# Kernel optimization log

Measured on AMD Instinct MI355X. Metric: run time of the kernel, lower is better.

The kernel has to match this reference:

```python
import jax, jax.numpy as jnp
import numpy as np

N_NODES = 100000
N_EDGES = 1600000
F_IN, F_HID, F_OUT = 512, 128, 64


def add_self_loops(edge_index, num_nodes):
    loop = jnp.arange(num_nodes, dtype=edge_index.dtype)
    loops = jnp.stack([loop, loop])  # [2, N]
    return jnp.concatenate([edge_index, loops], axis=1)


def gcn_conv(x, edge_index_sl, W, b, num_nodes):
    # x: [N, F_in], edge_index_sl: [2, E+N] (self-loops included)
    h = x @ W  # [N, F_out] transform before propagation (PyG GCNConv order)
    src, dst = edge_index_sl[0], edge_index_sl[1]
    ones = jnp.ones(src.shape[0], dtype=h.dtype)
    deg = jax.ops.segment_sum(ones, dst, num_segments=num_nodes)  # in-degree w/ self-loops
    dinv = jnp.where(deg > 0, jax.lax.rsqrt(deg), 0.0)
    norm = dinv[src] * dinv[dst]  # [E+N] symmetric normalization
    msg = h[src] * norm[:, None]  # gather + scale
    out = jax.ops.segment_sum(msg, dst, num_segments=num_nodes)  # scatter-add
    return out + b


def setup_inputs() -> dict:
    key = jax.random.key(0)
    k = jax.random.split(key, 6)
    x = jax.random.normal(k[0], (N_NODES, F_IN), dtype=jnp.float32)
    edge_index = jax.random.randint(k[1], (2, N_EDGES), 0, N_NODES, dtype=jnp.int64)
    W1 = jax.random.normal(k[2], (F_IN, F_HID), dtype=jnp.float32) * (1.0 / np.sqrt(F_IN))
    b1 = jnp.zeros((F_HID,), dtype=jnp.float32)
    W2 = jax.random.normal(k[3], (F_HID, F_OUT), dtype=jnp.float32) * (1.0 / np.sqrt(F_HID))
    b2 = jnp.zeros((F_OUT,), dtype=jnp.float32)
    return {"x": x, "edge_index": edge_index, "W1": W1, "b1": b1, "W2": W2, "b2": b2}


def reference(x, edge_index, W1, b1, W2, b2):
    ei = add_self_loops(edge_index, N_NODES)
    h = jax.nn.relu(gcn_conv(x, ei, W1, b1, N_NODES))
    out = gcn_conv(h, ei, W2, b2, N_NODES)
    return out
```

## Files before the change

### kernel.cpp

```cpp
#include <hip/hip_runtime.h>

#define N_NODES 100000
#define N_EDGES 1600000
#define F_IN 512
#define F_HID 128
#define F_OUT 64

#define BSH 8
#define NBUK 391

typedef unsigned int u32;
typedef __attribute__((ext_vector_type(8))) short bf16x8;
typedef __attribute__((ext_vector_type(4))) float f32x4;

__device__ float g7_bf2f(unsigned short u) {
    return __uint_as_float(((unsigned int)u) << 16);
}

__device__ unsigned short g7_f2bf(float f) {
    unsigned int u = __float_as_uint(f);
    u = u + 0x7fffu + ((u >> 16) & 1u);
    return (unsigned short)(u >> 16);
}

__device__ float2 g7_up(unsigned int u) {
    float2 r;
    r.x = __uint_as_float(u << 16);
    r.y = __uint_as_float(u & 0xffff0000u);
    return r;
}

__device__ static inline void g7_gl2lds16(const void* g, void* l) {
    __builtin_amdgcn_global_load_lds(
        (const __attribute__((address_space(1))) u32*)g,
        (__attribute__((address_space(3))) u32*)l, 16, 0, 0);
}

__global__ void GCN_16716012716713_kernel() {}

__global__ void g7_zero(int* p, int n) {
    int i = blockIdx.x * blockDim.x + threadIdx.x;
    if (i < n) p[i] = 0;
}

__global__ void g7_iprobe(const int* raw, int* iflag) {
    __shared__ int s[256];
    int tid = threadIdx.x;
    int f = 0;
    for (int i = tid; i < 1024; i += 256) {
        if (raw[2 * i + 1] != 0) f = 1;
    }
    s[tid] = f;
    __syncthreads();
    for (int off = 128; off > 0; off >>= 1) {
        if (tid < off) s[tid] |= s[tid + off];
        __syncthreads();
    }
    if (tid == 0) iflag[0] = s[0];
}

__global__ void g7_fprobe(const unsigned int* xw, int* fflag) {
    __shared__ int s[256];
    int tid = threadIdx.x;
    int cnt = 0;
    for (int i = tid; i < 4096; i += 256) {
        unsigned int lo = xw[i] & 0xffffu;
        unsigned int e = (lo >> 7) & 0xffu;
        if (e >= 110u && e <= 140u) cnt = cnt + 1;
    }
    s[tid] = cnt;
    __syncthreads();
    for (int off = 128; off > 0; off >>= 1) {
        if (tid < off) s[tid] += s[tid + off];
        __syncthreads();
    }
    if (tid == 0) fflag[0] = (s[0] > 2048) ? 1 : 0;
}

__global__ void g7_pack(const int* raw, const int* iflag, int* ei, int* deg) {
    int i = blockIdx.x * blockDim.x + threadIdx.x;
    if (i < 2 * N_EDGES) {
        int v;
        if (iflag[0] == 0) {
            v = raw[2 * i];
        } else {
            v = raw[i];
        }
        ei[i] = v;
        if (i >= N_EDGES) atomicAdd(&deg[v], 1);
    }
}

__global__ void g7_prep(const void* W1, const void* W2, const void* b1, const void* b2,
                        const int* fflag, unsigned short* W1Th, unsigned short* W1Tl,
                        float* W2f, float* b1f, float* b2f) {
    int i = blockIdx.x * blockDim.x + threadIdx.x;
    int isbf = fflag[0];
    if (i < F_IN * F_HID) {
        int k = i >> 7;
        int n = i & 127;
        float w;
        if (isbf == 1) {
            w = g7_bf2f(((const unsigned short*)W1)[i]);
        } else {
            w = ((const float*)W1)[i];
        }
        unsigned short hi = g7_f2bf(w);
        unsigned short lo = g7_f2bf(w - g7_bf2f(hi));
        W1Th[n * F_IN + k] = hi;
        W1Tl[n * F_IN + k] = lo;
    } else if (i < F_IN * F_HID + F_HID * F_OUT) {
        int j = i - F_IN * F_HID;
        W2f[j] = (isbf == 1) ? g7_bf2f(((const unsigned short*)W2)[j])
                             : ((const float*)W2)[j];
    } else if (i < F_IN * F_HID + F_HID * F_OUT + F_HID) {
        int j = i - F_IN * F_HID - F_HID * F_OUT;
        b1f[j] = (isbf == 1) ? g7_bf2f(((const unsigned short*)b1)[j])
                             : ((const float*)b1)[j];
    } else if (i < F_IN * F_HID + F_HID * F_OUT + F_HID + F_OUT) {
        int j = i - F_IN * F_HID - F_HID * F_OUT - F_HID;
        b2f[j] = (isbf == 1) ? g7_bf2f(((const unsigned short*)b2)[j])
                             : ((const float*)b2)[j];
    }
}

__global__ void g7_dinv(const int* deg, float* dinv) {
    int i = blockIdx.x * blockDim.x + threadIdx.x;
    if (i < N_NODES) {
        dinv[i] = rsqrtf((float)deg[i] + 1.0f);
    }
}

__global__ void g7_bsum(const int* deg, int* bsum) {
    __shared__ int s[256];
    int i = blockIdx.x * 256 + threadIdx.x;
    s[threadIdx.x] = (i < N_NODES) ? deg[i] : 0;
    __syncthreads();
    for (int off = 128; off > 0; off >>= 1) {
        if (threadIdx.x < off) s[threadIdx.x] += s[threadIdx.x + off];
        __syncthreads();
    }
    if (threadIdx.x == 0) bsum[blockIdx.x] = s[0];
}

__global__ void g7_bscan(const int* bsum, int* boff, int nblk, int* rowptr) {
    __shared__ int s[512];
    int tid = threadIdx.x;
    int v = (tid < nblk) ? bsum[tid] : 0;
    s[tid] = v;
    __syncthreads();
    for (int off = 1; off < 512; off <<= 1) {
        int t = (tid >= off) ? s[tid - off] : 0;
        __syncthreads();
        s[tid] += t;
        __syncthreads();
    }
    if (tid < nblk) boff[tid] = s[tid] - v;
    if (tid == nblk - 1) rowptr[N_NODES] = s[tid];
}

__global__ void g7_scan(const int* deg, const int* boff, int* rowptr) {
    __shared__ int s[256];
    int i = blockIdx.x * 256 + threadIdx.x;
    int v = (i < N_NODES) ? deg[i] : 0;
    s[threadIdx.x] = v;
    __syncthreads();
    for (int off = 1; off < 256; off <<= 1) {
        int t = (threadIdx.x >= off) ? s[threadIdx.x - off] : 0;
        __syncthreads();
        s[threadIdx.x] += t;
        __syncthreads();
    }
    if (i < N_NODES) {
        rowptr[i] = s[threadIdx.x] - v + boff[blockIdx.x];
    }
}

__global__ void g7_binit(const int* rowptr, int* bcur) {
    int b = blockIdx.x * blockDim.x + threadIdx.x;
    if (b < NBUK) bcur[b] = rowptr[b << BSH];
}

#define P1_EPT 32
#define P1_TILE (256 * P1_EPT)
__global__ void g7_part1(const int* ei, int* bcur, uint2* part) {
    __shared__ int cnt[NBUK + 1];
    __shared__ int base[NBUK + 1];
    int tid = threadIdx.x;
    long long t0 = (long long)blockIdx.x * P1_TILE;
    for (int i = tid; i < NBUK; i += 256) cnt[i] = 0;
    __syncthreads();
#pragma unroll 4
    for (int r = 0; r < P1_EPT; ++r) {
        long long e = t0 + r * 256 + tid;
        if (e < N_EDGES) {
            int d = ei[N_EDGES + e];
            atomicAdd(&cnt[d >> BSH], 1);
        }
    }
    __syncthreads();
    for (int i = tid; i < NBUK; i += 256) {
        int c = cnt[i];
        base[i] = (c > 0) ? atomicAdd(&bcur[i], c) : 0;
        cnt[i] = 0;
    }
    __syncthreads();
#pragma unroll 4
    for (int r = 0; r < P1_EPT; ++r) {
        long long e = t0 + r * 256 + tid;
        if (e < N_EDGES) {
            int s = ei[e];
            int d = ei[N_EDGES + e];
            int bk = d >> BSH;
            int off = atomicAdd(&cnt[bk], 1);
            uint2 p; p.x = (u32)s; p.y = (u32)d;
            part[(long long)base[bk] + off] = p;
        }
    }
}

__global__ void g7_part2(const int* rowptr, const uint2* part, int* csr) {
    __shared__ int lcur[256];
    int b = blockIdx.x;
    int tid = threadIdx.x;
    int n0 = b << BSH;
    int n1 = n0 + 256; if (n1 > N_NODES) n1 = N_NODES;
    if (tid < 256) {
        int node = n0 + tid;
        lcur[tid] = (node < N_NODES) ? rowptr[node] : 0;
    }
    __syncthreads();
    int beg = rowptr[n0];
    int end = rowptr[n1];
    for (int j = beg + tid; j < end; j += 512) {
        uint2 p = part[j];
        int pos = atomicAdd(&lcur[p.y - n0], 1);
        csr[pos] = (int)p.x;
    }
}

__global__ __launch_bounds__(512, 4) void g7_gemm1s(const void* x, const int* fflag,
        const unsigned short* W1Th, const unsigned short* W1Tl, unsigned short* h1b) {
    __shared__ uint4 smv[4096];
    char* smc = (char*)smv;
    int tid = threadIdx.x;
    int m0 = blockIdx.x * 128;
    int w = tid >> 6;
    int lane = tid & 63;
    int wr = w >> 2, wc = w & 3;
    int la = lane & 15;
    int lk = lane >> 4;
    int isbf = fflag[0];
    int ar = tid >> 2;
    int ah = tid & 3;

    f32x4 acc[4][2];
#pragma unroll
    for (int i = 0; i < 4; ++i)
#pragma unroll
        for (int j = 0; j < 2; ++j) acc[i][j] = (f32x4){0.f, 0.f, 0.f, 0.f};

    uint4 rA[2];

    auto loadA = [&](int k0) {
        int m = m0 + ar;
        if (m >= N_NODES) m = N_NODES - 1;
        if (isbf) {
            const char* s = (const char*)x + ((long long)m * F_IN + k0 + ah * 8) * 2;
            rA[0] = *(const uint4*)s;
        } else {
            const char* s = (const char*)x + ((long long)m * F_IN + k0 + ah * 8) * 4;
            rA[0] = *(const uint4*)s;
            rA[1] = *(const uint4*)(s + 16);
        }
    };

    auto writeA = [&](char* As) {
        float f[8];
        if (isbf) {
            const unsigned short* p = (const unsigned short*)&rA[0];
#pragma unroll
            for (int j = 0; j < 8; ++j) f[j] = g7_bf2f(p[j]);
        } else {
            const float* p = (const float*)rA;
#pragma unroll
            for (int j = 0; j < 8; ++j) f[j] = p[j];
        }
        unsigned int hw[4], lw[4];
#pragma unroll
        for (int j = 0; j < 4; ++j) {
            unsigned short h0 = g7_f2bf(f[2 * j]);
            unsigned short h1v = g7_f2bf(f[2 * j + 1]);
            unsigned short l0 = g7_f2bf(f[2 * j] - g7_bf2f(h0));
            unsigned short l1 = g7_f2bf(f[2 * j + 1] - g7_bf2f(h1v));
            hw[j] = (unsigned int)h0 | ((unsigned int)h1v << 16);
            lw[j] = (unsigned int)l0 | ((unsigned int)l1 << 16);
        }
        int swz = (ar & 7) << 4;
        char* dst = As + ar * 128;
        *(uint4*)(dst + ((ah * 16) ^ swz))      = make_uint4(hw[0], hw[1], hw[2], hw[3]);
        *(uint4*)(dst + ((64 + ah * 16) ^ swz)) = make_uint4(lw[0], lw[1], lw[2], lw[3]);
    };

    auto stageB = [&](char* Bs, int k0) {
#pragma unroll
        for (int p = 0; p < 2; ++p) {
            int nr = w * 16 + p * 8 + (lane >> 3);
            int cp = ((lane & 7) * 16) ^ (((lane >> 3) & 7) << 4);
            const char* src = (cp < 64)
                ? (const char*)W1Th + (long long)nr * 1024 + k0 * 2 + cp
                : (const char*)W1Tl + (long long)nr * 1024 + k0 * 2 + (cp - 64);
            g7_gl2lds16(src, Bs + (w * 16 + p * 8) * 128);
        }
    };

    auto compute = [&](const char* As, const char* Bs) {
        bf16x8 bh[2], bl[2];
#pragma unroll
        for (int j = 0; j < 2; ++j) {
            int n = wc * 32 + j * 16 + la;
            int swzb = (n & 7) << 4;
            const char* bb = Bs + n * 128;
            bh[j] = *(const bf16x8*)(bb + ((lk * 16) ^ swzb));
            bl[j] = *(const bf16x8*)(bb + ((64 + lk * 16) ^ swzb));
        }
#pragma unroll
        for (int i = 0; i < 4; ++i) {
            int r = wr * 64 + i * 16 + la;
            int swz = (r & 7) << 4;
            const char* ab = As + r * 128;
            bf16x8 ah_ = *(const bf16x8*)(ab + ((lk * 16) ^ swz));
            bf16x8 al_ = *(const bf16x8*)(ab + ((64 + lk * 16) ^ swz));
#pragma unroll
            for (int j = 0; j < 2; ++j) {
                acc[i][j] = __builtin_amdgcn_mfma_f32_16x16x32_bf16(
                    ah_, bh[j], acc[i][j], 0, 0, 0);
                acc[i][j] = __builtin_amdgcn_mfma_f32_16x16x32_bf16(
                    al_, bh[j], acc[i][j], 0, 0, 0);
                acc[i][j] = __builtin_amdgcn_mfma_f32_16x16x32_bf16(
                    ah_, bl[j], acc[i][j], 0, 0, 0);
            }
        }
    };

    loadA(0);
    stageB(smc + 16384, 0);
    writeA(smc);
    __syncthreads();

    for (int kt = 0; kt < 16; ++kt) {
        char* bc = smc + (kt & 1) * 32768;
        char* bn = smc + ((kt & 1) ^ 1) * 32768;
        if (kt < 15) {
            loadA((kt + 1) * 32);
            stageB(bn + 16384, (kt + 1) * 32);
        }
        compute(bc, bc + 16384);
        if (kt < 15) writeA(bn);
        __syncthreads();
    }

#pragma unroll
    for (int i = 0; i < 4; ++i) {
#pragma unroll
        for (int j = 0; j < 2; ++j) {
            int n = wc * 32 + j * 16 + la;
#pragma unroll
            for (int q = 0; q < 4; ++q) {
                int m = m0 + wr * 64 + i * 16 + lk * 4 + q;
                if (m < N_NODES) {
                    h1b[(long long)m * F_HID + n] = g7_f2bf(acc[i][j][q]);
                }
            }
        }
    }
}

__global__ void g7_agg1(const int* rowptr, const int* csr, const float* dinv,
                        const unsigned short* h1b, const float* b1, float* r1) {
    int node = blockIdx.x * 4 + (threadIdx.x >> 6);
    int lane = threadIdx.x & 63;
    int g = lane >> 4;
    int fl = lane & 15;
    if (node >= N_NODES) return;
    int beg = rowptr[node];
    int end = rowptr[node + 1];
    const uint4* hv = (const uint4*)h1b;
    float a[8];
#pragma unroll
    for (int t = 0; t < 8; ++t) a[t] = 0.f;
    int j = beg + g;
    for (; j + 4 < end; j += 8) {
        int s0 = csr[j];
        int s1 = csr[j + 4];
        float w0 = dinv[s0];
        float w1 = dinv[s1];
        uint4 v0 = hv[(long long)s0 * 16 + fl];
        uint4 v1 = hv[(long long)s1 * 16 + fl];
        float2 p;
        p = g7_up(v0.x); a[0] += p.x * w0; a[1] += p.y * w0;
        p = g7_up(v0.y); a[2] += p.x * w0; a[3] += p.y * w0;
        p = g7_up(v0.z); a[4] += p.x * w0; a[5] += p.y * w0;
        p = g7_up(v0.w); a[6] += p.x * w0; a[7] += p.y * w0;
        p = g7_up(v1.x); a[0] += p.x * w1; a[1] += p.y * w1;
        p = g7_up(v1.y); a[2] += p.x * w1; a[3] += p.y * w1;
        p = g7_up(v1.z); a[4] += p.x * w1; a[5] += p.y * w1;
        p = g7_up(v1.w); a[6] += p.x * w1; a[7] += p.y * w1;
    }
    if (j < end) {
        int s0 = csr[j];
        float w0 = dinv[s0];
        uint4 v0 = hv[(long long)s0 * 16 + fl];
        float2 p;
        p = g7_up(v0.x); a[0] += p.x * w0; a[1] += p.y * w0;
        p = g7_up(v0.y); a[2] += p.x * w0; a[3] += p.y * w0;
        p = g7_up(v0.z); a[4] += p.x * w0; a[5] += p.y * w0;
        p = g7_up(v0.w); a[6] += p.x * w0; a[7] += p.y * w0;
    }
    float di = dinv[node];
    if (g == 0) {
        uint4 vd = hv[(long long)node * 16 + fl];
        float2 p;
        p = g7_up(vd.x); a[0] += p.x * di; a[1] += p.y * di;
        p = g7_up(vd.y); a[2] += p.x * di; a[3] += p.y * di;
        p = g7_up(vd.z); a[4] += p.x * di; a[5] += p.y * di;
        p = g7_up(vd.w); a[6] += p.x * di; a[7] += p.y * di;
    }
#pragma unroll
    for (int t = 0; t < 8; ++t) {
        a[t] += __shfl_xor(a[t], 16);
        a[t] += __shfl_xor(a[t], 32);
    }
    if (g == 0) {
        float4 b0 = *(const float4*)(b1 + 8 * fl);
        float4 b1v = *(const float4*)(b1 + 8 * fl + 4);
        float o[8];
        o[0] = a[0] * di + b0.x; o[1] = a[1] * di + b0.y;
        o[2] = a[2] * di + b0.z; o[3] = a[3] * di + b0.w;
        o[4] = a[4] * di + b1v.x; o[5] = a[5] * di + b1v.y;
        o[6] = a[6] * di + b1v.z; o[7] = a[7] * di + b1v.w;
#pragma unroll
        for (int t = 0; t < 8; ++t) if (o[t] < 0.f) o[t] = 0.f;
        float* dst = r1 + (long long)node * F_HID + 8 * fl;
        float4 s0; s0.x = o[0]; s0.y = o[1]; s0.z = o[2]; s0.w = o[3];
        float4 s1; s1.x = o[4]; s1.y = o[5]; s1.z = o[6]; s1.w = o[7];
        *(float4*)dst = s0;
        *(float4*)(dst + 4) = s1;
    }
}

__global__ void g7_gemm2(const float* r1, const float* W2, unsigned short* h2b) {
    __shared__ float Rs[32][68];
    __shared__ float Ws[32][64];
    int tid = threadIdx.x;
    int m0 = blockIdx.x * 64;
    int tx = tid & 15;
    int ty = tid >> 4;
    float acc[4][4];
#pragma unroll
    for (int i = 0; i < 4; ++i) {
#pragma unroll
        for (int j = 0; j < 4; ++j) acc[i][j] = 0.0f;
    }

    for (int k0 = 0; k0 < F_HID; k0 += 32) {
#pragma unroll
        for (int r = 0; r < 8; ++r) {
            int i = r * 256 + tid;
            int kk = i & 31;
            int mm = i >> 5;
            int m = m0 + mm;
            float v = 0.0f;
            if (m < N_NODES) {
                v = r1[(long long)m * F_HID + k0 + kk];
            }
            Rs[kk][mm] = v;
        }
#pragma unroll
        for (int r = 0; r < 8; ++r) {
            int i = r * 256 + tid;
            int wk = i >> 6;
            int wn = i & 63;
            Ws[wk][wn] = W2[(k0 + wk) * F_OUT + wn];
        }
        __syncthreads();
#pragma unroll
        for (int k = 0; k < 32; ++k) {
            float a[4];
            float b[4];
#pragma unroll
            for (int i = 0; i < 4; ++i) a[i] = Rs[k][ty * 4 + i];
#pragma unroll
            for (int j = 0; j < 4; ++j) b[j] = Ws[k][tx * 4 + j];
#pragma unroll
            for (int i = 0; i < 4; ++i) {
#pragma unroll
                for (int j = 0; j < 4; ++j) acc[i][j] += a[i] * b[j];
            }
        }
        __syncthreads();
    }
#pragma unroll
    for (int i = 0; i < 4; ++i) {
        int m = m0 + ty * 4 + i;
        if (m < N_NODES) {
            unsigned int w0 = (unsigned int)g7_f2bf(acc[i][0])
                            | ((unsigned int)g7_f2bf(acc[i][1]) << 16);
            unsigned int w1 = (unsigned int)g7_f2bf(acc[i][2])
                            | ((unsigned int)g7_f2bf(acc[i][3]) << 16);
            uint2 o; o.x = w0; o.y = w1;
            *(uint2*)(h2b + (long long)m * F_OUT + tx * 4) = o;
        }
    }
}

__global__ void g7_agg2(const int* rowptr, const int* csr, const float* dinv,
                        const unsigned short* h2b, const float* b2, const int* fflag,
                        void* out) {
    int node = blockIdx.x * 4 + (threadIdx.x >> 6);
    int lane = threadIdx.x & 63;
    int g = lane >> 3;
    int fl = lane & 7;
    if (node >= N_NODES) return;
    int beg = rowptr[node];
    int end = rowptr[node + 1];
    const uint4* hv = (const uint4*)h2b;
    float a[8];
#pragma unroll
    for (int t = 0; t < 8; ++t) a[t] = 0.f;
    int j = beg + g;
    for (; j + 8 < end; j += 16) {
        int s0 = csr[j];
        int s1 = csr[j + 8];
        float w0 = dinv[s0];
        float w1 = dinv[s1];
        uint4 v0 = hv[(long long)s0 * 8 + fl];
        uint4 v1 = hv[(long long)s1 * 8 + fl];
        float2 p;
        p = g7_up(v0.x); a[0] += p.x * w0; a[1] += p.y * w0;
        p = g7_up(v0.y); a[2] += p.x * w0; a[3] += p.y * w0;
        p = g7_up(v0.z); a[4] += p.x * w0; a[5] += p.y * w0;
        p = g7_up(v0.w); a[6] += p.x * w0; a[7] += p.y * w0;
        p = g7_up(v1.x); a[0] += p.x * w1; a[1] += p.y * w1;
        p = g7_up(v1.y); a[2] += p.x * w1; a[3] += p.y * w1;
        p = g7_up(v1.z); a[4] += p.x * w1; a[5] += p.y * w1;
        p = g7_up(v1.w); a[6] += p.x * w1; a[7] += p.y * w1;
    }
    if (j < end) {
        int s0 = csr[j];
        float w0 = dinv[s0];
        uint4 v0 = hv[(long long)s0 * 8 + fl];
        float2 p;
        p = g7_up(v0.x); a[0] += p.x * w0; a[1] += p.y * w0;
        p = g7_up(v0.y); a[2] += p.x * w0; a[3] += p.y * w0;
        p = g7_up(v0.z); a[4] += p.x * w0; a[5] += p.y * w0;
        p = g7_up(v0.w); a[6] += p.x * w0; a[7] += p.y * w0;
    }
    float di = dinv[node];
    if (g == 0) {
        uint4 vd = hv[(long long)node * 8 + fl];
        float2 p;
        p = g7_up(vd.x); a[0] += p.x * di; a[1] += p.y * di;
        p = g7_up(vd.y); a[2] += p.x * di; a[3] += p.y * di;
        p = g7_up(vd.z); a[4] += p.x * di; a[5] += p.y * di;
        p = g7_up(vd.w); a[6] += p.x * di; a[7] += p.y * di;
    }
#pragma unroll
    for (int t = 0; t < 8; ++t) {
        a[t] += __shfl_xor(a[t], 8);
        a[t] += __shfl_xor(a[t], 16);
        a[t] += __shfl_xor(a[t], 32);
    }
    if (g == 0) {
        float o[8];
#pragma unroll
        for (int t = 0; t < 8; ++t) o[t] = a[t] * di + b2[8 * fl + t];
        long long oi = (long long)node * F_OUT + 8 * fl;
        if (fflag[0] == 1) {
            unsigned int w0 = (u32)g7_f2bf(o[0]) | ((u32)g7_f2bf(o[1]) << 16);
            unsigned int w1 = (u32)g7_f2bf(o[2]) | ((u32)g7_f2bf(o[3]) << 16);
            unsigned int w2 = (u32)g7_f2bf(o[4]) | ((u32)g7_f2bf(o[5]) << 16);
            unsigned int w3 = (u32)g7_f2bf(o[6]) | ((u32)g7_f2bf(o[7]) << 16);
            *(uint4*)((unsigned short*)out + oi) = make_uint4(w0, w1, w2, w3);
        } else {
            float* dst = (float*)out + oi;
            float4 s0; s0.x = o[0]; s0.y = o[1]; s0.z = o[2]; s0.w = o[3];
            float4 s1; s1.x = o[4]; s1.y = o[5]; s1.z = o[6]; s1.w = o[7];
            *(float4*)dst = s0;
            *(float4*)(dst + 4) = s1;
        }
    }
}

extern "C" void kernel_launch(void* const* d_in, const int* in_sizes, int n_in,
                              void* d_out, int out_size, void* d_ws, size_t ws_size,
                              hipStream_t stream) {
    const void* x     = d_in[0];
    const int* ei_raw = (const int*)d_in[1];
    const void* W1    = d_in[2];
    const void* b1    = d_in[3];
    const void* W2    = d_in[4];
    const void* b2    = d_in[5];

    const int NBLK = (N_NODES + 255) / 256;

    char* ws = (char*)d_ws;
    int*   deg    = (int*)(ws + 0);
    int*   iflag  = (int*)(ws + 409600);
    int*   fflag  = (int*)(ws + 409616);
    int*   bsum   = (int*)(ws + 409632);
    int*   boff   = (int*)(ws + 412800);
    int*   bcur   = (int*)(ws + 450560);
    float* dinv   = (float*)(ws + 524288);
    unsigned short* W1Th = (unsigned short*)(ws + 1048576);
    unsigned short* W1Tl = (unsigned short*)(ws + 1179648);
    float* b1f    = (float*)(ws + 1310720);
    float* W2f    = (float*)(ws + 1311232);
    float* b2f    = (float*)(ws + 1344000);
    int*   ei     = (int*)(ws + 2097152);
    int*   rowptr = (int*)(ws + 14897152);
    int*   csr    = (int*)(ws + 16777216);
    unsigned short* h1b = (unsigned short*)(ws + 23177216);
    uint2* part   = (uint2*)(ws + 50331648);
    float* r1     = (float*)(ws + 74377216);
    unsigned short* h2b = (unsigned short*)(ws + 125577216);

    g7_zero<<<(N_NODES + 255) / 256, 256, 0, stream>>>(deg, N_NODES);

    g7_iprobe<<<1, 256, 0, stream>>>(ei_raw, iflag);
    g7_fprobe<<<1, 256, 0, stream>>>((const unsigned int*)x, fflag);

    g7_pack<<<(2 * N_EDGES + 255) / 256, 256, 0, stream>>>(ei_raw, iflag, ei, deg);

    const int PREP_N = F_IN * F_HID + F_HID * F_OUT + F_HID + F_OUT;
    g7_prep<<<(PREP_N + 255) / 256, 256, 0, stream>>>(W1, W2, b1, b2, fflag,
                                                      W1Th, W1Tl, W2f, b1f, b2f);

    g7_dinv<<<(N_NODES + 255) / 256, 256, 0, stream>>>(deg, dinv);

    g7_bsum<<<NBLK, 256, 0, stream>>>(deg, bsum);
    g7_bscan<<<1, 512, 0, stream>>>(bsum, boff, NBLK, rowptr);
    g7_scan<<<NBLK, 256, 0, stream>>>(deg, boff, rowptr);

    g7_binit<<<(NBUK + 255) / 256, 256, 0, stream>>>(rowptr, bcur);
    g7_part1<<<(N_EDGES + P1_TILE - 1) / P1_TILE, 256, 0, stream>>>(ei, bcur, part);
    g7_part2<<<NBUK, 512, 0, stream>>>(rowptr, part, csr);

    g7_gemm1s<<<(N_NODES + 127) / 128, 512, 0, stream>>>(x, fflag, W1Th, W1Tl, h1b);

    g7_agg1<<<N_NODES / 4, 256, 0, stream>>>(rowptr, csr, dinv, h1b, b1f, r1);

    g7_gemm2<<<(N_NODES + 63) / 64, 256, 0, stream>>>(r1, W2f, h2b);

    g7_agg2<<<N_NODES / 4, 256, 0, stream>>>(rowptr, csr, dinv, h2b, b2f, fflag, d_out);
}
```

Before: 609.3 us.

## Move second GEMM onto MFMA with split-bf16 operands and double-buffered LDS

Replaces the scalar FP32 shared-memory tiled GEMM for layer 2 with an MFMA 16x16x32 bf16 kernel. It splits both operands into hi/lo bf16 parts and uses three MFMAs to keep close to fp32 accuracy. W2 is now pre-transposed and split in the prep kernel, A tiles are converted in registers and written to swizzled LDS, and the K loop is double-buffered with async global-to-LDS loads for B. The output store becomes scalar 16-bit writes, which may be less coalesced than the old vector stores.

```diff
diff --git a/kernel.cpp b/kernel.cpp
--- a/kernel.cpp
+++ b/kernel.cpp
@@ -93,7 +93,8 @@
 
 __global__ void g7_prep(const void* W1, const void* W2, const void* b1, const void* b2,
                         const int* fflag, unsigned short* W1Th, unsigned short* W1Tl,
-                        float* W2f, float* b1f, float* b2f) {
+                        unsigned short* W2Th, unsigned short* W2Tl,
+                        float* b1f, float* b2f) {
     int i = blockIdx.x * blockDim.x + threadIdx.x;
     int isbf = fflag[0];
     if (i < F_IN * F_HID) {
@@ -111,8 +112,18 @@
         W1Tl[n * F_IN + k] = lo;
     } else if (i < F_IN * F_HID + F_HID * F_OUT) {
         int j = i - F_IN * F_HID;
-        W2f[j] = (isbf == 1) ? g7_bf2f(((const unsigned short*)W2)[j])
-                             : ((const float*)W2)[j];
+        int k = j >> 6;
+        int n = j & 63;
+        float w;
+        if (isbf == 1) {
+            w = g7_bf2f(((const unsigned short*)W2)[j]);
+        } else {
+            w = ((const float*)W2)[j];
+        }
+        unsigned short hi = g7_f2bf(w);
+        unsigned short lo = g7_f2bf(w - g7_bf2f(hi));
+        W2Th[n * F_HID + k] = hi;
+        W2Tl[n * F_HID + k] = lo;
     } else if (i < F_IN * F_HID + F_HID * F_OUT + F_HID) {
         int j = i - F_IN * F_HID - F_HID * F_OUT;
         b1f[j] = (isbf == 1) ? g7_bf2f(((const unsigned short*)b1)[j])
@@ -449,67 +460,128 @@
     }
 }
 
-__global__ void g7_gemm2(const float* r1, const float* W2, unsigned short* h2b) {
-    __shared__ float Rs[32][68];
-    __shared__ float Ws[32][64];
+__global__ __launch_bounds__(256, 2) void g7_gemm2m(const float* r1,
+        const unsigned short* W2Th, const unsigned short* W2Tl, unsigned short* h2b) {
+    __shared__ uint4 smv[3072];
+    char* smc = (char*)smv;
     int tid = threadIdx.x;
-    int m0 = blockIdx.x * 64;
-    int tx = tid & 15;
-    int ty = tid >> 4;
-    float acc[4][4];
+    int m0 = blockIdx.x * 128;
+    int w = tid >> 6;
+    int lane = tid & 63;
+    int wr = w >> 1, wc = w & 1;
+    int la = lane & 15;
+    int lk = lane >> 4;
+    int ar = tid >> 1;
+    int ah = tid & 1;
+
+    f32x4 acc[4][2];
+#pragma unroll
+    for (int i = 0; i < 4; ++i)
+#pragma unroll
+        for (int j = 0; j < 2; ++j) acc[i][j] = (f32x4){0.f, 0.f, 0.f, 0.f};
+
+    uint4 rA[4];
+
+    auto loadA = [&](int k0) {
+        int m = m0 + ar;
+        if (m >= N_NODES) m = N_NODES - 1;
+        const char* s = (const char*)(r1 + (long long)m * F_HID + k0 + ah * 16);
+        rA[0] = *(const uint4*)s;
+        rA[1] = *(const uint4*)(s + 16);
+        rA[2] = *(const uint4*)(s + 32);
+        rA[3] = *(const uint4*)(s + 48);
+    };
+
+    auto writeA = [&](char* As) {
+        const float* f = (const float*)rA;
+        unsigned int hw[8], lw[8];
+#pragma unroll
+        for (int j = 0; j < 8; ++j) {
+            unsigned short h0 = g7_f2bf(f[2 * j]);
+            unsigned short h1v = g7_f2bf(f[2 * j + 1]);
+            unsigned short l0 = g7_f2bf(f[2 * j] - g7_bf2f(h0));
+            unsigned short l1 = g7_f2bf(f[2 * j + 1] - g7_bf2f(h1v));
+            hw[j] = (unsigned int)h0 | ((unsigned int)h1v << 16);
+            lw[j] = (unsigned int)l0 | ((unsigned int)l1 << 16);
+        }
+        int swz = (ar & 7) << 4;
+        char* dst = As + ar * 128;
+        *(uint4*)(dst + ((ah * 32 + 0) ^ swz))      = make_uint4(hw[0], hw[1], hw[2], hw[3]);
+        *(uint4*)(dst + ((ah * 32 + 16) ^ swz))     = make_uint4(hw[4], hw[5], hw[6], hw[7]);
+        *(uint4*)(dst + ((64 + ah * 32 + 0) ^ swz)) = make_uint4(lw[0], lw[1], lw[2], lw[3]);
+        *(uint4*)(dst + ((64 + ah * 32 + 16) ^ swz))= make_uint4(lw[4], lw[5], lw[6], lw[7]);
+    };
+
+    auto stageB = [&](char* Bs, int k0) {
+#pragma unroll
+        for (int p = 0; p < 2; ++p) {
+            int nr = w * 16 + p * 8 + (lane >> 3);
+            int cp = ((lane & 7) * 16) ^ (((lane >> 3) & 7) << 4);
+            const char* src = (cp < 64)
+                ? (const char*)W2Th + (long long)nr * 256 + k0 * 2 + cp
+                : (const char*)W2Tl + (long long)nr * 256 + k0 * 2 + (cp - 64);
+            g7_gl2lds16(src, Bs + (w * 16 + p * 8) * 128);
+        }
+    };
+
+    auto compute = [&](const char* As, const char* Bs) {
+        bf16x8 bh[2], bl[2];
+#pragma unroll
+        for (int j = 0; j < 2; ++j) {
+            int n = wc * 32 + j * 16 + la;
+            int swzb = (n & 7) << 4;
+            const char* bb = Bs + n * 128;
+            bh[j] = *(const bf16x8*)(bb + ((lk * 16) ^ swzb));
+            bl[j] = *(const bf16x8*)(bb + ((64 + lk * 16) ^ swzb));
+        }
+#pragma unroll
+        for (int i = 0; i < 4; ++i) {
+            int r = wr * 64 + i * 16 + la;
+            int swz = (r & 7) << 4;
+            const char* ab = As + r * 128;
+            bf16x8 ah_ = *(const bf16x8*)(ab + ((lk * 16) ^ swz));
+            bf16x8 al_ = *(const bf16x8*)(ab + ((64 + lk * 16) ^ swz));
+#pragma unroll
+            for (int j = 0; j < 2; ++j) {
+                acc[i][j] = __builtin_amdgcn_mfma_f32_16x16x32_bf16(
+                    ah_, bh[j], acc[i][j], 0, 0, 0);
+                acc[i][j] = __builtin_amdgcn_mfma_f32_16x16x32_bf16(
+                    al_, bh[j], acc[i][j], 0, 0, 0);
+                acc[i][j] = __builtin_amdgcn_mfma_f32_16x16x32_bf16(
+                    ah_, bl[j], acc[i][j], 0, 0, 0);
+            }
+        }
+    };
+
+    loadA(0);
+    stageB(smc + 16384, 0);
+    writeA(smc);
+    __syncthreads();
+
+    for (int kt = 0; kt < 4; ++kt) {
+        char* bc = smc + (kt & 1) * 24576;
+        char* bn = smc + ((kt & 1) ^ 1) * 24576;
+        if (kt < 3) {
+            loadA((kt + 1) * 32);
+            stageB(bn + 16384, (kt + 1) * 32);
+        }
+        compute(bc, bc + 16384);
+        if (kt < 3) writeA(bn);
+        __syncthreads();
+    }
+
 #pragma unroll
     for (int i = 0; i < 4; ++i) {
 #pragma unroll
-        for (int j = 0; j < 4; ++j) acc[i][j] = 0.0f;
-    }
-
-    for (int k0 = 0; k0 < F_HID; k0 += 32) {
-#pragma unroll
-        for (int r = 0; r < 8; ++r) {
-            int i = r * 256 + tid;
-            int kk = i & 31;
-            int mm = i >> 5;
-            int m = m0 + mm;
-            float v = 0.0f;
-            if (m < N_NODES) {
-                v = r1[(long long)m * F_HID + k0 + kk];
+        for (int j = 0; j < 2; ++j) {
+            int n = wc * 32 + j * 16 + la;
+#pragma unroll
+            for (int q = 0; q < 4; ++q) {
+                int m = m0 + wr * 64 + i * 16 + lk * 4 + q;
+                if (m < N_NODES) {
+                    h2b[(long long)m * F_OUT + n] = g7_f2bf(acc[i][j][q]);
+                }
             }
-            Rs[kk][mm] = v;
-        }
-#pragma unroll
-        for (int r = 0; r < 8; ++r) {
-            int i = r * 256 + tid;
-            int wk = i >> 6;
-            int wn = i & 63;
-            Ws[wk][wn] = W2[(k0 + wk) * F_OUT + wn];
-        }
-        __syncthreads();
-#pragma unroll
-        for (int k = 0; k < 32; ++k) {
-            float a[4];
-            float b[4];
-#pragma unroll
-            for (int i = 0; i < 4; ++i) a[i] = Rs[k][ty * 4 + i];
-#pragma unroll
-            for (int j = 0; j < 4; ++j) b[j] = Ws[k][tx * 4 + j];
-#pragma unroll
-            for (int i = 0; i < 4; ++i) {
-#pragma unroll
-                for (int j = 0; j < 4; ++j) acc[i][j] += a[i] * b[j];
-            }
-        }
-        __syncthreads();
-    }
-#pragma unroll
-    for (int i = 0; i < 4; ++i) {
-        int m = m0 + ty * 4 + i;
-        if (m < N_NODES) {
-            unsigned int w0 = (unsigned int)g7_f2bf(acc[i][0])
-                            | ((unsigned int)g7_f2bf(acc[i][1]) << 16);
-            unsigned int w1 = (unsigned int)g7_f2bf(acc[i][2])
-                            | ((unsigned int)g7_f2bf(acc[i][3]) << 16);
-            uint2 o; o.x = w0; o.y = w1;
-            *(uint2*)(h2b + (long long)m * F_OUT + tx * 4) = o;
         }
     }
 }
@@ -615,7 +687,8 @@
     unsigned short* W1Th = (unsigned short*)(ws + 1048576);
     unsigned short* W1Tl = (unsigned short*)(ws + 1179648);
     float* b1f    = (float*)(ws + 1310720);
-    float* W2f    = (float*)(ws + 1311232);
+    unsigned short* W2Th = (unsigned short*)(ws + 1311232);
+    unsigned short* W2Tl = (unsigned short*)(ws + 1327616);
     float* b2f    = (float*)(ws + 1344000);
     int*   ei     = (int*)(ws + 2097152);
     int*   rowptr = (int*)(ws + 14897152);
@@ -634,7 +707,7 @@
 
     const int PREP_N = F_IN * F_HID + F_HID * F_OUT + F_HID + F_OUT;
     g7_prep<<<(PREP_N + 255) / 256, 256, 0, stream>>>(W1, W2, b1, b2, fflag,
-                                                      W1Th, W1Tl, W2f, b1f, b2f);
+                                                      W1Th, W1Tl, W2Th, W2Tl, b1f, b2f);
 
     g7_dinv<<<(N_NODES + 255) / 256, 256, 0, stream>>>(deg, dinv);
 
@@ -650,7 +723,7 @@
 
     g7_agg1<<<N_NODES / 4, 256, 0, stream>>>(rowptr, csr, dinv, h1b, b1f, r1);
 
-    g7_gemm2<<<(N_NODES + 63) / 64, 256, 0, stream>>>(r1, W2f, h2b);
+    g7_gemm2m<<<(N_NODES + 127) / 128, 256, 0, stream>>>(r1, W2Th, W2Tl, h2b);
 
     g7_agg2<<<N_NODES / 4, 256, 0, stream>>>(rowptr, csr, dinv, h2b, b2f, fflag, d_out);
 }
```

Result: faster. 588.0 us (-3.5%).
